# Performance work log

Hardware: AMD Instinct MI355X
Metric: run time of the kernel (lower is better)

## Reference

```python
import jax, jax.numpy as jnp
import numpy as np

N_NODES = 80000; N_EDGES = 480000; F_IN = 5; DIM = 3; HID = 128; LAT = 128
N_POOLS = 2; RATIO = 0.5; SLOPE = 0.2  # GATv2 leaky_relu negative slope


def _p(key, shape, fan_in):
    return jax.random.normal(key, shape, dtype=jnp.float32) / np.sqrt(float(fan_in))


def setup_inputs() -> dict:
    key = jax.random.key(0)
    ks = jax.random.split(key, 20)
    c0 = F_IN + DIM + 3          # conv0 in-channels: x | pos | y*ones
    ch = HID + DIM               # all later convs / pool gnns: h | pos
    return dict(
        x=jax.random.normal(ks[0], (N_NODES, F_IN), dtype=jnp.float32),
        y=jax.random.normal(ks[1], (1,), dtype=jnp.float32),
        pos=jax.random.normal(ks[2], (N_NODES, DIM), dtype=jnp.float32),
        edge_index=jax.random.randint(ks[3], (2, N_EDGES), 0, N_NODES),
        Wl0=_p(ks[4], (c0, HID), c0), Wr0=_p(ks[5], (c0, HID), c0),
        We0=_p(ks[6], (DIM, HID), DIM), a0=_p(ks[7], (HID,), HID), b0=jnp.zeros((HID,), jnp.float32),
        # stacked convs: [conv1, pool-conv1, pool-conv2, last-conv], all (HID+DIM)->HID(=LAT)
        Wls=_p(ks[8], (4, ch, HID), ch), Wrs=_p(ks[9], (4, ch, HID), ch),
        Wes=_p(ks[10], (4, DIM, HID), DIM), atts=_p(ks[11], (4, HID), HID), bs=jnp.zeros((4, HID), jnp.float32),
        # SAGPool score GNNs: (HID+DIM)->1
        pWl=_p(ks[12], (N_POOLS, ch, 1), ch), pWr=_p(ks[13], (N_POOLS, ch, 1), ch),
        pWe=_p(ks[14], (N_POOLS, DIM, 1), DIM), pa=_p(ks[15], (N_POOLS, 1), 1), pb=jnp.zeros((N_POOLS, 1), jnp.float32),
        linW=_p(ks[16], (LAT, LAT), LAT), linb=jnp.zeros((LAT,), jnp.float32),
    )


def _gatv2(xf, ei, ea, Wl, Wr, We, att, b):
    # PyG GATv2Conv, heads=1, add_self_loops=True, fill_value='mean' for loop edge_attr
    N = xf.shape[0]
    src = jnp.asarray(ei[0]); dst = jnp.asarray(ei[1])
    ones = jnp.ones((src.shape[0],), dtype=xf.dtype)
    deg = jax.ops.segment_sum(ones, dst, num_segments=N)
    loop_attr = jax.ops.segment_sum(ea, dst, num_segments=N) / jnp.clip(deg, 1.0)[:, None]
    ar = jnp.arange(N)
    src_f = jnp.concatenate([src, ar]); dst_f = jnp.concatenate([dst, ar])
    ea_f = jnp.concatenate([ea, loop_attr], axis=0)
    xl = xf @ Wl; xr = xf @ Wr                              # [N, C]
    m = jax.nn.leaky_relu(xl[src_f] + xr[dst_f] + ea_f @ We, SLOPE)  # [Ef, C]
    logits = m @ att                                        # [Ef]
    mx = jax.ops.segment_max(logits, dst_f, num_segments=N)
    z = jnp.exp(logits - mx[dst_f])
    denom = jax.ops.segment_sum(z, dst_f, num_segments=N)
    alpha = z / denom[dst_f]
    return jax.ops.segment_sum(alpha[:, None] * xl[src_f], dst_f, num_segments=N) + b


def _augment(ei, N):
    # adj + adj@adj (sparse coo with coalesce): union of 1-hop and 2-hop edges
    s, t = ei[0].astype(np.int64), ei[1].astype(np.int64)
    order = np.argsort(s, kind='stable')
    t2 = t[order]
    counts = np.bincount(s, minlength=N)
    starts = np.concatenate([[0], np.cumsum(counts)[:-1]])
    lens = counts[t]                      # out-degree of each edge's target (middle node)
    total = int(lens.sum())
    within = np.arange(total) - np.repeat(np.cumsum(lens) - lens, lens)
    b = t2[np.repeat(starts[t], lens) + within]
    a = np.repeat(s, lens)
    key = np.unique(np.concatenate([s * N + t, a * N + b]))
    return np.stack([key // N, key % N])


def _filter_adj(ei, perm, N):
    mask = np.zeros(N, dtype=bool); mask[perm] = True
    keep = mask[ei[0]] & mask[ei[1]]
    relabel = np.full(N, -1, dtype=np.int64); relabel[perm] = np.arange(len(perm))
    return relabel[ei[:, keep]]


def _encoder(fl, ei0, structs):
    (x, y, pos, Wl0, Wr0, We0, a0, b0, Wls, Wrs, Wes, atts, bs,
     pWl, pWr, pWe, pa, pb, linW, linb) = fl
    capture = structs is None
    recs = []
    ei = ei0
    ea = pos[ei[1]] - pos[ei[0]]
    h = jax.nn.elu(_gatv2(jnp.concatenate([x, pos, y * jnp.ones_like(pos)], 1), ei, ea, Wl0, Wr0, We0, a0, b0))
    h = jax.nn.elu(_gatv2(jnp.concatenate([h, pos], 1), ei, ea, Wls[0], Wrs[0], Wes[0], atts[0], bs[0]))
    pe = [ei]; pp = [pos]; eas = [ea]
    N = x.shape[0]
    for l in range(N_POOLS):
        ei_aug = _augment(np.asarray(ei), N) if capture else structs[l][0]
        ea_aug = pos[ei_aug[1]] - pos[ei_aug[0]]
        score = jnp.tanh(_gatv2(jnp.concatenate([h, pos], 1), ei_aug, ea_aug,
                                pWl[l], pWr[l], pWe[l], pa[l], pb[l])[:, 0])
        k = int(np.ceil(RATIO * N))
        if capture:
            _, perm = jax.lax.top_k(score, k)
            perm = np.asarray(perm)
            ei_next = _filter_adj(np.asarray(ei), perm, N)
            recs.append((ei_aug, perm, ei_next))
        else:
            _, perm, ei_next = structs[l]
        h = h[perm] * score[perm][:, None]
        pos = pos[perm]
        ei = ei_next; N = k
        ea = pos[ei[1]] - pos[ei[0]]
        pe.insert(0, ei); pp.insert(0, pos); eas.insert(0, ea)
        h = jax.nn.elu(_gatv2(jnp.concatenate([h, pos], 1), ei, ea,
                              Wls[l + 1], Wrs[l + 1], Wes[l + 1], atts[l + 1], bs[l + 1]))
    h = jax.nn.elu(_gatv2(jnp.concatenate([h, pos], 1), ei, ea, Wls[3], Wrs[3], Wes[3], atts[3], bs[3]))
    out = h @ linW + linb   # torch.vmap(self.lin)
    return out, pe, pp, eas, recs


def reference(x, y, pos, edge_index, Wl0, Wr0, We0, a0, b0, Wls, Wrs, Wes, atts, bs,
              pWl, pWr, pWe, pa, pb, linW, linb):
    fl = (x, y, pos, Wl0, Wr0, We0, a0, b0, Wls, Wrs, Wes, atts, bs,
          pWl, pWr, pWe, pa, pb, linW, linb)
    out, pe, pp, eas, _ = _encoder(fl, np.asarray(edge_index), None)
    return (out,) + tuple(jnp.asarray(e) for e in pe) + tuple(pp) + tuple(eas)
```

## Files before the change

### kernel.cpp

```cpp
#include <hip/hip_runtime.h>

typedef unsigned long long ull;

#define NN0 80000
#define EE0 480000
#define KK1 40000
#define KK2 20000
#define FLATMAX 8000000
#define SCH 4096
#define CDIV(a,b) (((a)+(b)-1)/(b))
#define HBINS (1<<21)
#define LSW 1024
#define FCAP 512
#define JCAP 8

#define C_E1 2
#define C_E2 3
#define C_M0 5
#define C_M1 6

__device__ __forceinline__ int getE(const int* p, int s){ if(!p) return s; int e=*p; return e<s? e : s; }
__device__ __forceinline__ float leakyf(float x){ return x>0.f? x : 0.2f*x; }
__device__ __forceinline__ double leakyd(double x){ return x>0.0? x : 0.2*x; }
__device__ __forceinline__ float eluf(float x){ return x>0.f? x : (expf(x)-1.f); }

__device__ __forceinline__ ull encd(double f){ ull u=(ull)__double_as_longlong(f); return (u>>63)? ~u : (u|0x8000000000000000ULL); }

template<int MODE, bool DUAL>
__global__ void gemm_k(const float* __restrict__ F1, const float* __restrict__ pos,
                       const float* __restrict__ yv,
                       const float* __restrict__ W1, const float* __restrict__ W2,
                       const float* __restrict__ bias,
                       float* __restrict__ O1, float* __restrict__ O2, int N)
{
  const int K = MODE==0? 11 : (MODE==1? 131 : 128);
  __shared__ float lf[32][132];
  int t = threadIdx.x;
  int row0 = blockIdx.x*32;

  if(MODE==0){
    for(int i=t;i<32*11;i+=256){
      int r=i/11, k=i-r*11; int row=row0+r;
      float f=0.f;
      if(row<N) f = (k<5)? F1[(size_t)row*5+k] : (k<8? pos[(size_t)row*3+(k-5)] : yv[0]);
      lf[r][k]=f;
    }
  } else {
    for(int i=t;i<32*32;i+=256){
      int r=i>>5, c4=i&31; int row=row0+r;
      float4 v; v.x=0.f;v.y=0.f;v.z=0.f;v.w=0.f;
      if(row<N) v = *(const float4*)(F1+(size_t)row*128+c4*4);
      *(float4*)(&lf[r][c4*4]) = v;
    }
    if(MODE==1){
      for(int i=t;i<32*3;i+=256){
        int r=i/3, d=i-r*3; int row=row0+r;
        lf[r][128+d] = (row<N)? pos[(size_t)row*3+d] : 0.f;
      }
    }
  }
  __syncthreads();

  int cg = t&31, rg = t>>5;
  int g = cg*4;
  int rbase = rg*4;

  float acc1[4][4]; float acc2[4][4];
  #pragma unroll
  for(int rr=0;rr<4;rr++)
    #pragma unroll
    for(int c=0;c<4;c++){ acc1[rr][c]=0.f; acc2[rr][c]=0.f; }

  #pragma unroll 4
  for(int k=0;k<K;k++){
    float4 w = *(const float4*)(W1 + (size_t)k*128 + g);
    float4 v; v.x=0.f;v.y=0.f;v.z=0.f;v.w=0.f;
    if(DUAL) v = *(const float4*)(W2 + (size_t)k*128 + g);
    #pragma unroll
    for(int rr=0;rr<4;rr++){
      float f = lf[rbase+rr][k];
      acc1[rr][0]+=f*w.x; acc1[rr][1]+=f*w.y; acc1[rr][2]+=f*w.z; acc1[rr][3]+=f*w.w;
      if(DUAL){ acc2[rr][0]+=f*v.x; acc2[rr][1]+=f*v.y; acc2[rr][2]+=f*v.z; acc2[rr][3]+=f*v.w; }
    }
  }

  float4 bb; bb.x=0.f;bb.y=0.f;bb.z=0.f;bb.w=0.f;
  if(bias) bb = *(const float4*)(bias+g);
  #pragma unroll
  for(int rr=0;rr<4;rr++){
    int row = row0 + rbase + rr;
    if(row<N){
      float4 r1; r1.x=acc1[rr][0]+bb.x; r1.y=acc1[rr][1]+bb.y; r1.z=acc1[rr][2]+bb.z; r1.w=acc1[rr][3]+bb.w;
      *(float4*)(O1+(size_t)row*128+g) = r1;
      if(DUAL){
        float4 r2; r2.x=acc2[rr][0]; r2.y=acc2[rr][1]; r2.z=acc2[rr][2]; r2.w=acc2[rr][3];
        *(float4*)(O2+(size_t)row*128+g) = r2;
      }
    }
  }
}

__global__ void scan_p1(const int* __restrict__ in, const int* pN, int Ns, int* __restrict__ bsums){
  __shared__ int red[256];
  int n = getE(pN,Ns);
  int base = blockIdx.x*SCH;
  int s=0;
  for(int i=base+threadIdx.x; i<base+SCH; i+=256) if(i<n) s+=in[i];
  red[threadIdx.x]=s; __syncthreads();
  for(int o=128;o;o>>=1){ if(threadIdx.x<(unsigned)o) red[threadIdx.x]+=red[threadIdx.x+o]; __syncthreads(); }
  if(threadIdx.x==0) bsums[blockIdx.x]=red[0];
}
__global__ void scan_p2(int* bsums, int nb){
  __shared__ int lds[256];
  int t=threadIdx.x;
  int v = (t<nb)? bsums[t] : 0;
  lds[t]=v; __syncthreads();
  for(int o=1;o<256;o<<=1){ int u=0; if(t>=o) u=lds[t-o]; __syncthreads(); lds[t]+=u; __syncthreads(); }
  if(t<nb) bsums[t]=lds[t]-v;
}
__global__ void scan_p3(const int* __restrict__ in, int* __restrict__ out, const int* pN, int Ns,
                        const int* __restrict__ bsums, int* total){
  __shared__ int tsum[256];
  int n = getE(pN,Ns);
  int base = blockIdx.x*SCH + threadIdx.x*16;
  int v[16]; int s=0;
  #pragma unroll
  for(int q=0;q<16;q++){ int i=base+q; int xv=(i<n)? in[i]:0; v[q]=s; s+=xv; }
  tsum[threadIdx.x]=s; __syncthreads();
  int mine=s;
  for(int o=1;o<256;o<<=1){ int u=0; if(threadIdx.x>=(unsigned)o) u=tsum[threadIdx.x-o]; __syncthreads(); tsum[threadIdx.x]+=u; __syncthreads(); }
  int pre = bsums[blockIdx.x] + tsum[threadIdx.x] - mine;
  #pragma unroll
  for(int q=0;q<16;q++){
    int i=base+q;
    if(i<=n){
      int val = pre+v[q];
      out[i]=val;
      if(i==n && total) *total=val;
    }
  }
}

__global__ void fscan_p1(const int* __restrict__ es, const int* __restrict__ ed, const int* pE, int Es,
                         const int* __restrict__ rank, int k, int* __restrict__ bsums){
  __shared__ int red[256];
  int n = getE(pE,Es);
  int base = blockIdx.x*SCH;
  int s=0;
  for(int i=base+threadIdx.x; i<base+SCH; i+=256)
    if(i<n) s += (rank[es[i]]<k && rank[ed[i]]<k) ? 1 : 0;
  red[threadIdx.x]=s; __syncthreads();
  for(int o=128;o;o>>=1){ if(threadIdx.x<(unsigned)o) red[threadIdx.x]+=red[threadIdx.x+o]; __syncthreads(); }
  if(threadIdx.x==0) bsums[blockIdx.x]=red[0];
}
__global__ void fscan_p3(const int* __restrict__ es, const int* __restrict__ ed, const int* pE, int Es,
                         const int* __restrict__ rank, int k, const int* __restrict__ bsums,
                         int* __restrict__ ns, int* __restrict__ nd, int* total){
  __shared__ int tsum[256];
  int n = getE(pE,Es);
  int base = blockIdx.x*SCH + threadIdx.x*16;
  int v[16]; int rs[16], rd[16]; unsigned fm=0; int s=0;
  #pragma unroll
  for(int q=0;q<16;q++){
    int i=base+q; int xv=0;
    if(i<n){
      int a=rank[es[i]], b=rank[ed[i]];
      rs[q]=a; rd[q]=b;
      if(a<k && b<k){ xv=1; fm |= 1u<<q; }
    }
    v[q]=s; s+=xv;
  }
  tsum[threadIdx.x]=s; __syncthreads();
  int mine=s;
  for(int o=1;o<256;o<<=1){ int u=0; if(threadIdx.x>=(unsigned)o) u=tsum[threadIdx.x-o]; __syncthreads(); tsum[threadIdx.x]+=u; __syncthreads(); }
  int pre = bsums[blockIdx.x] + tsum[threadIdx.x] - mine;
  #pragma unroll
  for(int q=0;q<16;q++){
    int i=base+q;
    if(i<n && ((fm>>q)&1u)){
      int p = pre+v[q];
      ns[p]=rs[q]; nd[p]=rd[q];
    }
    if(i==n && total) *total = pre+v[q];
  }
}

__global__ void count_src(const int* __restrict__ es, const int* pE, int Es, int* cnts){
  int e = blockIdx.x*256+threadIdx.x; int E = getE(pE,Es); if(e>=E) return;
  atomicAdd(&cnts[es[e]], 1);
}
__global__ void fill_eord(const int* __restrict__ es, const int* __restrict__ ed, const int* pE, int Es,
                          const int* __restrict__ dstarts, int* cursor, int* insrc){
  int e = blockIdx.x*256+threadIdx.x; int E = getE(pE,Es); if(e>=E) return;
  int d = ed[e];
  int p = dstarts[d] + atomicAdd(&cursor[d],1);
  insrc[p] = es[e];
}

__global__ void feat_fused(const int* __restrict__ insrc, const int* __restrict__ dstarts,
                           const float* __restrict__ A, const float* __restrict__ B,
                           const float* __restrict__ pos,
                           const float* __restrict__ We, const float* __restrict__ att,
                           const float* __restrict__ bias, float* __restrict__ h, int N)
{
  __shared__ float lgAll[4][FCAP];
  int wv = threadIdx.x>>6, lane = threadIdx.x&63;
  int w = blockIdx.x*4 + wv;
  bool active = (w<N);
  if(!active) w = N-1;
  float* lg = lgAll[wv];
  int r0=dstarts[w], r1=dstarts[w+1]; int din=r1-r0;
  int c=lane, c2=lane+64;
  float B0 = B[(size_t)w*128+c], B1 = B[(size_t)w*128+c2];
  float We0c=We[c], We1c=We[128+c], We2c=We[256+c];
  float We0d=We[c2], We1d=We[128+c2], We2d=We[256+c2];
  float attc=att[c], attd=att[c2];
  float pw0=pos[w*3], pw1=pos[w*3+1], pw2=pos[w*3+2];

  float ra0[JCAP], ra1[JCAP];
  float l0=0,l1=0,l2=0;
  for(int jb=0;jb<din;jb+=JCAP){
    #pragma unroll
    for(int u=0;u<JCAP;u++){
      int j=jb+u;
      if(j<din){
        int s = insrc[r0+j];
        float e0=pw0-pos[s*3], e1=pw1-pos[s*3+1], e2=pw2-pos[s*3+2];
        l0+=e0; l1+=e1; l2+=e2;
        float a0=A[(size_t)s*128+c], a1=A[(size_t)s*128+c2];
        if(jb==0){ ra0[u]=a0; ra1[u]=a1; }
        float m1 = a0 + B0 + e0*We0c + e1*We1c + e2*We2c;
        float m2 = a1 + B1 + e0*We0d + e1*We1d + e2*We2d;
        float p = leakyf(m1)*attc + leakyf(m2)*attd;
        for(int o=32;o;o>>=1) p += __shfl_down(p,o,64);
        if(lane==0 && j<FCAP) lg[j]=p;
      }
    }
  }
  float inv = 1.f/fmaxf((float)din, 1.f);
  float q0=l0*inv, q1=l1*inv, q2=l2*inv;
  float a0w=A[(size_t)w*128+c], a1w=A[(size_t)w*128+c2];
  float pself;
  {
    float m1 = a0w + B0 + q0*We0c + q1*We1c + q2*We2c;
    float m2 = a1w + B1 + q0*We0d + q1*We1d + q2*We2d;
    float p = leakyf(m1)*attc + leakyf(m2)*attd;
    for(int o=32;o;o>>=1) p += __shfl_down(p,o,64);
    pself = __shfl(p,0,64);
  }
  float mx = pself;
  int dc = din<FCAP? din : FCAP;
  for(int j=lane;j<dc;j+=64) mx = fmaxf(mx, lg[j]);
  for(int o=32;o;o>>=1) mx = fmaxf(mx, __shfl_down(mx,o,64));
  mx = __shfl(mx,0,64);
  for(int j=FCAP;j<din;j++){
    int s = insrc[r0+j];
    float e0=pw0-pos[s*3], e1=pw1-pos[s*3+1], e2=pw2-pos[s*3+2];
    float a0=A[(size_t)s*128+c], a1=A[(size_t)s*128+c2];
    float m1 = a0 + B0 + e0*We0c + e1*We1c + e2*We2c;
    float m2 = a1 + B1 + e0*We0d + e1*We1d + e2*We2d;
    float p = leakyf(m1)*attc + leakyf(m2)*attd;
    for(int o=32;o;o>>=1) p += __shfl_down(p,o,64);
    p = __shfl(p,0,64);
    mx = fmaxf(mx, p);
  }

  float denom=0.f, acc0=0.f, acc1=0.f;
  for(int jb=0;jb<din;jb+=JCAP){
    #pragma unroll
    for(int u=0;u<JCAP;u++){
      int j=jb+u;
      if(j<din){
        float a0,a1; int s=-1;
        if(jb==0){ a0=ra0[u]; a1=ra1[u]; }
        else {
          s = insrc[r0+j];
          a0=A[(size_t)s*128+c]; a1=A[(size_t)s*128+c2];
        }
        float lgj;
        if(j<FCAP) lgj = lg[j];
        else {
          float e0=pw0-pos[s*3], e1=pw1-pos[s*3+1], e2=pw2-pos[s*3+2];
          float m1 = a0 + B0 + e0*We0c + e1*We1c + e2*We2c;
          float m2 = a1 + B1 + e0*We0d + e1*We1d + e2*We2d;
          float p = leakyf(m1)*attc + leakyf(m2)*attd;
          for(int o=32;o;o>>=1) p += __shfl_down(p,o,64);
          lgj = __shfl(p,0,64);
        }
        float z = expf(lgj - mx);
        denom += z;
        acc0 += z*a0;
        acc1 += z*a1;
      }
    }
  }
  {
    float z = expf(pself - mx);
    denom += z;
    acc0 += z*a0w; acc1 += z*a1w;
  }
  float iv = 1.f/denom;
  float b0v=bias[c], b1v=bias[c2];
  acc0 = eluf(acc0*iv + b0v); acc1 = eluf(acc1*iv + b1v);
  if(active){
    h[(size_t)w*128+c ] = acc0;
    h[(size_t)w*128+c2] = acc1;
  }
}

__global__ void gemm_score(const float* __restrict__ h, const float* __restrict__ pos,
                           const float* __restrict__ pWl, const float* __restrict__ pWr,
                           double* __restrict__ xls, double* __restrict__ xrs, int N)
{
  int t = threadIdx.x;
  int lane = t&31;
  int n = blockIdx.x*8 + (t>>5);
  if(n>=N) return;
  double sl=0, sr=0;
  #pragma unroll
  for(int q=0;q<4;q++){
    int k = lane + q*32;
    double f = (double)h[(size_t)n*128+k];
    sl += f*(double)pWl[k]; sr += f*(double)pWr[k];
  }
  if(lane<3){
    double f = (double)pos[n*3+lane];
    sl += f*(double)pWl[128+lane]; sr += f*(double)pWr[128+lane];
  }
  for(int o=16;o;o>>=1){ sl += __shfl_down(sl,o,32); sr += __shfl_down(sr,o,32); }
  if(lane==0){ xls[n]=sl; xrs[n]=sr; }
}

__global__ void score_fused2(const int* __restrict__ insrc, const int* __restrict__ dstarts,
                             const float* __restrict__ pos,
                             const double* __restrict__ xls, const double* __restrict__ xrs,
                             const float* __restrict__ pWe, const float* __restrict__ paP,
                             const float* __restrict__ pbP,
                             double* __restrict__ score, ull* __restrict__ ek, int N)
{
  __shared__ int lsAll[4][LSW];
  int wv = threadIdx.x>>6;
  int lane = threadIdx.x&63;
  int w = blockIdx.x*4 + wv;
  bool active = (w<N);
  if(!active) w = N-1;
  int* ls = lsAll[wv];
  int r0=dstarts[w], r1=dstarts[w+1]; int din=r1-r0;
  for(int j=lane;j<din && j<LSW;j+=64) ls[j]=insrc[r0+j];
  __syncthreads();
  int off = din<LSW? din : LSW;
  for(int base=0; base<din && base<LSW; base+=64){
    int t = base + lane;
    int u0=0, len=0;
    if(t<din && t<LSW){
      int u = ls[t];
      u0 = dstarts[u]; len = dstarts[u+1]-u0;
    }
    int pre = len;
    #pragma unroll
    for(int o=1;o<64;o<<=1){ int v=__shfl_up(pre,o,64); if(lane>=o) pre+=v; }
    int tot = __shfl(pre, 63, 64);
    int myoff = off + pre - len;
    for(int j=0;j<len;j++){ int p=myoff+j; if(p<LSW) ls[p]=insrc[u0+j]; }
    off += tot;
  }
  int d = off<LSW? off : LSW;
  __syncthreads();

  float pd0=pos[w*3], pd1=pos[w*3+1], pd2=pos[w*3+2];
  double w0=(double)pWe[0], w1=(double)pWe[1], w2=(double)pWe[2], pa=(double)paP[0];
  double xrd=xrs[w];
  ull umask=0;
  double lgv[4], xv[4];
  double mx=-1e300, s0=0,s1=0,s2=0; int ucnt=0;
  #pragma unroll
  for(int it=0; it<4; it++){
    int j = lane + it*64;
    if(j<d){
      int s = ls[j];
      bool uniq = true;
      for(int q=0;q<j;q++) if(ls[q]==s){ uniq=false; break; }
      if(uniq){
        umask |= 1ULL<<it;
        ucnt++;
        double e0=(double)(pd0-pos[s*3]), e1=(double)(pd1-pos[s*3+1]), e2=(double)(pd2-pos[s*3+2]);
        s0+=e0; s1+=e1; s2+=e2;
        double xl = xls[s];
        double lg = leakyd(xl+xrd + e0*w0+e1*w1+e2*w2) * pa;
        lgv[it]=lg; xv[it]=xl;
        mx = fmax(mx, lg);
      }
    }
  }
  int nb=4;
  for(int j=lane+256; j<d; j+=64, nb++){
    int s = ls[j];
    bool uniq = true;
    for(int q=0;q<j;q++) if(ls[q]==s){ uniq=false; break; }
    if(uniq){
      umask |= 1ULL<<nb;
      ucnt++;
      double e0=(double)(pd0-pos[s*3]), e1=(double)(pd1-pos[s*3+1]), e2=(double)(pd2-pos[s*3+2]);
      s0+=e0; s1+=e1; s2+=e2;
      double lg = leakyd(xls[s]+xrd + e0*w0+e1*w1+e2*w2) * pa;
      mx = fmax(mx, lg);
    }
  }
  for(int o=32;o;o>>=1){
    mx = fmax(mx, __shfl_down(mx,o,64));
    s0 += __shfl_down(s0,o,64);
    s1 += __shfl_down(s1,o,64);
    s2 += __shfl_down(s2,o,64);
    ucnt += __shfl_down(ucnt,o,64);
  }
  mx=__shfl(mx,0,64); s0=__shfl(s0,0,64); s1=__shfl(s1,0,64); s2=__shfl(s2,0,64); ucnt=__shfl(ucnt,0,64);
  double invd = 1.0/(double)(ucnt>0? ucnt : 1);
  double lg_self = leakyd(xls[w]+xrd + (s0*invd)*w0 + (s1*invd)*w1 + (s2*invd)*w2) * pa;
  mx = fmax(mx, lg_self);
  double den=0, acc=0;
  #pragma unroll
  for(int it=0; it<4; it++){
    if((umask>>it)&1ULL){
      double z = exp(lgv[it]-mx);
      den += z; acc += z*xv[it];
    }
  }
  nb=4;
  for(int j=lane+256; j<d; j+=64, nb++){
    if((umask>>nb)&1ULL){
      int s = ls[j];
      double e0=(double)(pd0-pos[s*3]), e1=(double)(pd1-pos[s*3+1]), e2=(double)(pd2-pos[s*3+2]);
      double lg = leakyd(xls[s]+xrd + e0*w0+e1*w1+e2*w2) * pa;
      double z = exp(lg-mx);
      den += z; acc += z*xls[s];
    }
  }
  for(int o=32;o;o>>=1){
    den += __shfl_down(den,o,64);
    acc += __shfl_down(acc,o,64);
  }
  if(lane==0 && active){
    double z = exp(lg_self-mx);
    den += z; acc += z*xls[w];
    double sc = tanh(acc/den + (double)pbP[0]);
    score[w] = sc;
    ek[w] = encd(sc);
  }
}

__global__ void hist_g(const ull* __restrict__ ek, int N, int shift, const ull* __restrict__ selT,
                       int* __restrict__ hist){
  int i = blockIdx.x*256+threadIdx.x; if(i>=N) return;
  ull key = ek[i];
  if(shift+21 < 64){
    if((key >> (shift+21)) != ((*selT) >> (shift+21))) return;
  }
  atomicAdd(&hist[(int)((key>>shift)&0x1FFFFF)], 1);
}
__global__ void part21(const int* __restrict__ hist, int* __restrict__ partial){
  __shared__ int red[256];
  int b = blockIdx.x;
  int s=0;
  for(int i=threadIdx.x;i<1024;i+=256) s += hist[b*1024+i];
  red[threadIdx.x]=s; __syncthreads();
  for(int o=128;o;o>>=1){ if(threadIdx.x<(unsigned)o) red[threadIdx.x]+=red[threadIdx.x+o]; __syncthreads(); }
  if(threadIdx.x==0) partial[b]=red[0];
}
__global__ void findbin_g(const int* __restrict__ partial, const int* __restrict__ hist,
                          ull* __restrict__ selT, int* __restrict__ selRB, int k, int shift){
  __shared__ int ts[256];
  __shared__ int cstar, rbase;
  int t=threadIdx.x;
  int keff = k - *selRB;
  int s8[8]; int mysum=0;
  #pragma unroll
  for(int q=0;q<8;q++){ s8[q]=partial[t*8+q]; mysum+=s8[q]; }
  ts[t]=mysum; __syncthreads();
  for(int o=1;o<256;o<<=1){ int u=(t+o<256)? ts[t+o]:0; __syncthreads(); ts[t]+=u; __syncthreads(); }
  int after = (t<255)? ts[t+1] : 0;
  if(ts[t] >= keff && after < keff){
    int run = after;
    for(int q=7;q>=0;q--){
      if(run < keff && run + s8[q] >= keff){ cstar = t*8+q; rbase = run; }
      run += s8[q];
    }
  }
  __syncthreads();
  int cs=cstar, rb=rbase;
  int b4[4]; int ms=0;
  #pragma unroll
  for(int q=0;q<4;q++){ b4[q]=hist[cs*1024 + t*4 + q]; ms+=b4[q]; }
  ts[t]=ms; __syncthreads();
  for(int o=1;o<256;o<<=1){ int u=(t+o<256)? ts[t+o]:0; __syncthreads(); ts[t]+=u; __syncthreads(); }
  int after2 = (t<255)? ts[t+1] : 0;
  if(rb+ts[t] >= keff && rb+after2 < keff){
    int run = rb+after2;
    for(int q=3;q>=0;q--){
      if(run < keff && run + b4[q] >= keff){
        *selT |= ((ull)(cs*1024 + t*4 + q)) << shift;
        *selRB = (k - keff) + run;
      }
      run += b4[q];
    }
  }
}
__global__ void rank_hist(const ull* __restrict__ ek, int N, const ull* __restrict__ selT,
                          int* __restrict__ hist){
  int i = blockIdx.x*256+threadIdx.x; if(i>=N) return;
  ull key = ek[i]; if(key < *selT) return;
  int dg = (int)((~key >> 43) & 0x1FFFFF);
  atomicAdd(&hist[dg], 1);
}
__global__ void binscan(const int* __restrict__ hist, const int* __restrict__ p2,
                        int* __restrict__ binstarts){
  __shared__ int ts[256];
  int b = blockIdx.x, t = threadIdx.x;
  int v[4]; int s=0;
  #pragma unroll
  for(int q=0;q<4;q++){ v[q]=s; s+=hist[b*1024 + t*4 + q]; }
  ts[t]=s; __syncthreads();
  int mine=s;
  for(int o=1;o<256;o<<=1){ int u=0; if(t>=(unsigned)o) u=ts[t-o]; __syncthreads(); ts[t]+=u; __syncthreads(); }
  int pre = p2[b] + ts[t] - mine;
  #pragma unroll
  for(int q=0;q<4;q++) binstarts[b*1024 + t*4 + q] = pre + v[q];
  if(b==2047 && t==255) binstarts[HBINS] = p2[b] + ts[255];
}
__global__ void rank_fill(const ull* __restrict__ ek, int N, const ull* __restrict__ selT,
                          const int* __restrict__ binstarts, int* __restrict__ hist,
                          ull* __restrict__ mkeys, int* __restrict__ midx){
  int i = blockIdx.x*256+threadIdx.x; if(i>=N) return;
  ull key = ek[i]; if(key < *selT) return;
  int dg = (int)((~key >> 43) & 0x1FFFFF);
  int o = atomicSub(&hist[dg], 1) - 1;
  int p = binstarts[dg] + o;
  mkeys[p] = key; midx[p] = i;
}
__global__ void rank_within(const int* __restrict__ binstarts,
                            const ull* __restrict__ mkeys, const int* __restrict__ midx,
                            int* __restrict__ rank, int Nmax){
  int m = blockIdx.x*256+threadIdx.x; if(m>=Nmax) return;
  int total = binstarts[HBINS]; if(m>=total) return;
  ull key = mkeys[m]; int ii = midx[m];
  int dg = (int)((~key >> 43) & 0x1FFFFF);
  int s = binstarts[dg], e = binstarts[dg+1];
  int cnt = 0;
  for(int j=s;j<e;j++){
    ull kj = mkeys[j];
    cnt += (kj > key) || (kj == key && midx[j] < ii);
  }
  rank[ii] = s + cnt;
}
__global__ void scatter_perm(const int* __restrict__ rank, int N, int k, int* __restrict__ perm){
  int i = blockIdx.x*256+threadIdx.x; if(i>=N) return;
  int r = rank[i]; if(r<k) perm[r]=i;
}
__global__ void pool_gather(const float* __restrict__ h, const double* __restrict__ score,
                            const int* __restrict__ perm, int k, float* __restrict__ outA){
  int idx = blockIdx.x*256+threadIdx.x; if(idx>=k*32) return;
  int r = idx>>5, g = (idx&31)*4;
  int p = perm[r]; float sc = (float)score[p];
  const float4 x = *(const float4*)(h + (size_t)p*128 + g);
  float4 o; o.x=x.x*sc; o.y=x.y*sc; o.z=x.z*sc; o.w=x.w*sc;
  *(float4*)(outA + (size_t)r*128 + g) = o;
}
__global__ void pos_gather(const float* __restrict__ posc, const int* __restrict__ perm, int k, float* __restrict__ posn){
  int idx = blockIdx.x*256+threadIdx.x; if(idx>=k*3) return;
  int r = idx/3, j = idx-r*3;
  posn[idx] = posc[perm[r]*3+j];
}

__global__ void calc_offsets(const int* __restrict__ cnt, long long* __restrict__ offs){
  if(blockIdx.x==0 && threadIdx.x==0){
    long long E1 = cnt[C_E1], E2 = cnt[C_E2];
    long long o = (long long)KK2*128;
    offs[0]=0;
    offs[1]=o; o += 2*E2;
    offs[2]=o; o += 2*E1;
    offs[3]=o; o += 2*(long long)EE0;
    offs[4]=o; o += (long long)KK2*3;
    offs[5]=o; o += (long long)KK1*3;
    offs[6]=o; o += (long long)NN0*3;
    offs[7]=o; o += 3*E2;
    offs[8]=o; o += 3*E1;
    offs[9]=o;
  }
}
__global__ void emit3_pe(const int* __restrict__ s2, const int* __restrict__ d2, const int* pE2,
                         const int* __restrict__ s1, const int* __restrict__ d1, const int* pE1,
                         const int* __restrict__ s0, const int* __restrict__ d0,
                         const long long* __restrict__ offs, float* __restrict__ out){
  int e = blockIdx.x*256+threadIdx.x;
  int L = blockIdx.y;
  const int* s; const int* d; int E; int oi;
  if(L==0){ s=s2; d=d2; E=getE(pE2,EE0); oi=1; }
  else if(L==1){ s=s1; d=d1; E=getE(pE1,EE0); oi=2; }
  else { s=s0; d=d0; E=EE0; oi=3; }
  if(e>=E) return;
  long long o = offs[oi];
  out[o+e]   = (float)s[e];
  out[o+E+e] = (float)d[e];
}
__global__ void emit3_pp(const float* __restrict__ p2, const float* __restrict__ p1,
                         const float* __restrict__ p0,
                         const long long* __restrict__ offs, float* __restrict__ out){
  int i = blockIdx.x*256+threadIdx.x;
  int L = blockIdx.y;
  const float* p; int n; int oi;
  if(L==0){ p=p2; n=KK2*3; oi=4; }
  else if(L==1){ p=p1; n=KK1*3; oi=5; }
  else { p=p0; n=NN0*3; oi=6; }
  if(i>=n) return;
  out[offs[oi]+i] = p[i];
}
__global__ void emit3_eas(const int* __restrict__ s2, const int* __restrict__ d2, const int* pE2, const float* __restrict__ q2,
                          const int* __restrict__ s1, const int* __restrict__ d1, const int* pE1, const float* __restrict__ q1,
                          const int* __restrict__ s0, const int* __restrict__ d0, const float* __restrict__ q0,
                          const long long* __restrict__ offs, float* __restrict__ out){
  int e = blockIdx.x*256+threadIdx.x;
  int L = blockIdx.y;
  const int* s; const int* d; const float* pos; int E; int oi;
  if(L==0){ s=s2; d=d2; pos=q2; E=getE(pE2,EE0); oi=7; }
  else if(L==1){ s=s1; d=d1; pos=q1; E=getE(pE1,EE0); oi=8; }
  else { s=s0; d=d0; pos=q0; E=EE0; oi=9; }
  if(e>=E) return;
  long long o = offs[oi];
  int ss=s[e], dd=d[e];
  out[o+3*e+0] = pos[dd*3+0]-pos[ss*3+0];
  out[o+3*e+1] = pos[dd*3+1]-pos[ss*3+1];
  out[o+3*e+2] = pos[dd*3+2]-pos[ss*3+2];
}

extern "C" void kernel_launch(void* const* d_in, const int* in_sizes, int n_in,
                              void* d_out, int out_size, void* d_ws, size_t ws_size,
                              hipStream_t stream)
{
  const float* x    = (const float*)d_in[0];
  const float* yv   = (const float*)d_in[1];
  const float* pos0 = (const float*)d_in[2];
  const int*   ei   = (const int*)d_in[3];
  const float* Wl0  = (const float*)d_in[4];
  const float* Wr0  = (const float*)d_in[5];
  const float* We0  = (const float*)d_in[6];
  const float* a0   = (const float*)d_in[7];
  const float* b0   = (const float*)d_in[8];
  const float* Wls  = (const float*)d_in[9];
  const float* Wrs  = (const float*)d_in[10];
  const float* Wes  = (const float*)d_in[11];
  const float* atts = (const float*)d_in[12];
  const float* bs   = (const float*)d_in[13];
  const float* pWl  = (const float*)d_in[14];
  const float* pWr  = (const float*)d_in[15];
  const float* pWe  = (const float*)d_in[16];
  const float* pa   = (const float*)d_in[17];
  const float* pb   = (const float*)d_in[18];
  const float* linW = (const float*)d_in[19];
  const float* linb = (const float*)d_in[20];
  float* out = (float*)d_out;

  const int* eisrc = ei;
  const int* eidst = ei + EE0;

  char* base = (char*)d_ws; size_t off = 0;
  auto alloc = [&](size_t b)->void*{
    off = (off + 255) & ~(size_t)255;
    void* p = base + off; off += b; return p;
  };
  int*       cnt     = (int*)alloc(64*4);
  long long* offs    = (long long*)alloc(16*8);
  int*       bsums   = (int*)alloc(256*4);
  ull*       sel     = (ull*)alloc(2*8);
  int*       hist    = (int*)alloc((size_t)HBINS*4);
  int*       partial = (int*)alloc(2048*4);
  int*       partial2= (int*)alloc(2304*4);
  double*    xls     = (double*)alloc((size_t)NN0*8);
  double*    xrs     = (double*)alloc((size_t)NN0*8);
  double*    score   = (double*)alloc((size_t)NN0*8);
  ull*       ek      = (ull*)alloc((size_t)NN0*8);
  int*       rank    = (int*)alloc((size_t)NN0*4);
  int*       perm    = (int*)alloc((size_t)NN0*4);
  int*       cursor  = (int*)alloc((size_t)NN0*4);
  int*       ccnt    = (int*)alloc((size_t)NN0*4);
  int*       dstarts = (int*)alloc((size_t)(NN0+1)*4);
  int*       insrc   = (int*)alloc((size_t)EE0*4);
  int*       eb0s    = (int*)alloc((size_t)EE0*4);
  int*       eb0d    = (int*)alloc((size_t)EE0*4);
  int*       eb1s    = (int*)alloc((size_t)EE0*4);
  int*       eb1d    = (int*)alloc((size_t)EE0*4);
  float*     pos1    = (float*)alloc((size_t)KK1*12);
  float*     pos2    = (float*)alloc((size_t)KK2*12);
  float*     A       = (float*)alloc((size_t)NN0*128*4);
  float*     B       = (float*)alloc((size_t)NN0*128*4);
  float*     h       = (float*)alloc((size_t)NN0*128*4);
  void*      uni     = alloc((size_t)(EE0+FLATMAX)*8);
  if(off > ws_size) return;

  int*    binstarts= (int*)uni;
  ull*    mkeys    = (ull*)((int*)uni + (HBINS + 256));
  int*    midx     = (int*)(mkeys + NN0);
  ull*    selT  = sel;
  int*    selRB = (int*)(sel+1);

  hipMemsetAsync(cnt, 0, 64*4, stream);
  hipMemsetAsync(hist, 0, (size_t)HBINS*4, stream);

  auto scan = [&](const int* in, int* sout, const int* pN, int Ns, int* total){
    int nb = CDIV(Ns+1, SCH);
    scan_p1<<<nb,256,0,stream>>>(in,pN,Ns,bsums);
    scan_p2<<<1,256,0,stream>>>(bsums,nb);
    scan_p3<<<nb,256,0,stream>>>(in,sout,pN,Ns,bsums,total);
  };

  auto build_csr_dst = [&](const int* es, const int* ed, const int* pE, int Emax, int N){
    hipMemsetAsync(ccnt,0,(size_t)N*4,stream);
    count_src<<<CDIV(Emax,256),256,0,stream>>>(ed,pE,Emax,ccnt);
    scan(ccnt,dstarts,nullptr,N,nullptr);
    hipMemsetAsync(cursor,0,(size_t)N*4,stream);
    fill_eord<<<CDIV(Emax,256),256,0,stream>>>(es,ed,pE,Emax,dstarts,cursor,insrc);
  };

  auto feat_conv = [&](const float* Wl, const float* Wr, const float* We, const float* att, const float* bias,
                       int N, const float* pcur, bool conv0mode){
    if(conv0mode)
      gemm_k<0,true><<<CDIV(N,32),256,0,stream>>>(x,pcur,yv,Wl,Wr,nullptr,A,B,N);
    else
      gemm_k<1,true><<<CDIV(N,32),256,0,stream>>>(h,pcur,nullptr,Wl,Wr,nullptr,A,B,N);
    feat_fused<<<CDIV(N,4),256,0,stream>>>(insrc,dstarts,A,B,pcur,We,att,bias,h,N);
  };

  auto pool = [&](int l, int N, int k, const int* es, const int* ed, const int* pE, int Emax,
                  const float* pcur, float* pnext, int* ns, int* nd, int eslot){
    hipMemsetAsync(rank, 0x3f, (size_t)N*4, stream);
    gemm_score<<<CDIV(N,8),256,0,stream>>>(h,pcur,pWl+l*131,pWr+l*131,xls,xrs,N);
    score_fused2<<<CDIV(N,4),256,0,stream>>>(insrc,dstarts,pcur,xls,xrs,pWe+l*3,pa+l,pb+l,score,ek,N);
    hipMemsetAsync(sel,0,16,stream);
    for(int r=0;r<2;r++){
      int sh = 43 - 21*r;
      if(r>0) hipMemsetAsync(hist,0,(size_t)HBINS*4,stream);
      hist_g<<<CDIV(N,256),256,0,stream>>>(ek,N,sh,selT,hist);
      part21<<<2048,256,0,stream>>>(hist,partial);
      findbin_g<<<1,256,0,stream>>>(partial,hist,selT,selRB,k,sh);
    }
    hipMemsetAsync(hist,0,(size_t)HBINS*4,stream);
    rank_hist  <<<CDIV(N,256),256,0,stream>>>(ek,N,selT,hist);
    part21     <<<2048,256,0,stream>>>(hist,partial);
    scan(partial,partial2,nullptr,2048,nullptr);
    binscan    <<<2048,256,0,stream>>>(hist,partial2,binstarts);
    rank_fill  <<<CDIV(N,256),256,0,stream>>>(ek,N,selT,binstarts,hist,mkeys,midx);
    rank_within<<<CDIV(N,256),256,0,stream>>>(binstarts,mkeys,midx,rank,N);
    scatter_perm<<<CDIV(N,256),256,0,stream>>>(rank,N,k,perm);
    pool_gather<<<CDIV(k*32,256),256,0,stream>>>(h,score,perm,k,A);
    hipMemcpyAsync(h,A,(size_t)k*128*4,hipMemcpyDeviceToDevice,stream);
    pos_gather<<<CDIV(k*3,256),256,0,stream>>>(pcur,perm,k,pnext);
    {
      int nb = CDIV(Emax+1, SCH);
      fscan_p1<<<nb,256,0,stream>>>(es,ed,pE,Emax,rank,k,bsums);
      scan_p2<<<1,256,0,stream>>>(bsums,nb);
      fscan_p3<<<nb,256,0,stream>>>(es,ed,pE,Emax,rank,k,bsums,ns,nd,cnt+eslot);
    }
  };

  build_csr_dst(eisrc,eidst,nullptr,EE0, NN0);
  feat_conv(Wl0,Wr0,We0,a0,b0, NN0, pos0, true);
  feat_conv(Wls+0*16768,Wrs+0*16768,Wes+0*384,atts+0*128,bs+0*128, NN0, pos0, false);
  pool(0, NN0, KK1, eisrc,eidst,nullptr,EE0, pos0,pos1, eb0s,eb0d, C_E1);
  build_csr_dst(eb0s,eb0d,cnt+C_E1,EE0, KK1);
  feat_conv(Wls+1*16768,Wrs+1*16768,Wes+1*384,atts+1*128,bs+1*128, KK1, pos1, false);
  pool(1, KK1, KK2, eb0s,eb0d,cnt+C_E1,EE0, pos1,pos2, eb1s,eb1d, C_E2);
  build_csr_dst(eb1s,eb1d,cnt+C_E2,EE0, KK2);
  feat_conv(Wls+2*16768,Wrs+2*16768,Wes+2*384,atts+2*128,bs+2*128, KK2, pos2, false);
  feat_conv(Wls+3*16768,Wrs+3*16768,Wes+3*384,atts+3*128,bs+3*128, KK2, pos2, false);
  gemm_k<2,false><<<CDIV(KK2,32),256,0,stream>>>(h,nullptr,nullptr,linW,nullptr,linb,out,nullptr,KK2);

  calc_offsets<<<1,32,0,stream>>>(cnt,offs);
  {
    dim3 g(CDIV(EE0,256),3);
    emit3_pe <<<g,256,0,stream>>>(eb1s,eb1d,cnt+C_E2, eb0s,eb0d,cnt+C_E1, eisrc,eidst, offs,out);
    emit3_eas<<<g,256,0,stream>>>(eb1s,eb1d,cnt+C_E2,pos2, eb0s,eb0d,cnt+C_E1,pos1, eisrc,eidst,pos0, offs,out);
  }
  {
    dim3 g(CDIV(NN0*3,256),3);
    emit3_pp <<<g,256,0,stream>>>(pos2,pos1,pos0,offs,out);
  }
}
```

Before: 1.760 ms.

## Reuse first radix histogram for ranking bins and drop pooled-feature copy

The top-k selection now keeps the first-pass 21-bit histogram in its own buffer and uses a second buffer for the refinement pass. The bin-start scan is built directly from that first histogram in reverse order, which removes a separate rank_hist pass, its histogram memset and the multi-kernel scan. The pooled features are written straight into B and the next conv reads from B, so the device-to-device memcpy goes away. In exchange it adds an extra 8 MB histogram buffer, a memset of mkeys, and counts above-threshold items per bin using the full first-pass histogram, which relies on the selT filtering in rank_within to stay correct.

```diff
diff --git a/kernel.cpp b/kernel.cpp
--- a/kernel.cpp
+++ b/kernel.cpp
@@ -504,44 +504,55 @@
     }
   }
 }
-__global__ void rank_hist(const ull* __restrict__ ek, int N, const ull* __restrict__ selT,
-                          int* __restrict__ hist){
-  int i = blockIdx.x*256+threadIdx.x; if(i>=N) return;
-  ull key = ek[i]; if(key < *selT) return;
-  int dg = (int)((~key >> 43) & 0x1FFFFF);
-  atomicAdd(&hist[dg], 1);
-}
-__global__ void binscan(const int* __restrict__ hist, const int* __restrict__ p2,
-                        int* __restrict__ binstarts){
+__global__ void sufscan2048(const int* __restrict__ in, int* __restrict__ outcs){
   __shared__ int ts[256];
-  int b = blockIdx.x, t = threadIdx.x;
+  int t=threadIdx.x;
+  int v[8]; int s=0;
+  #pragma unroll
+  for(int q=7;q>=0;q--){ v[q]=s; s+=in[t*8+q]; }
+  ts[t]=s; __syncthreads();
+  int mine=s;
+  for(int o=1;o<256;o<<=1){ int u=(t+o<256)? ts[t+o]:0; __syncthreads(); ts[t]+=u; __syncthreads(); }
+  int post = ts[t] - mine;
+  #pragma unroll
+  for(int q=0;q<8;q++) outcs[t*8+q] = post + v[q];
+}
+__global__ void binscan_rev(const int* __restrict__ hist1, const int* __restrict__ csum,
+                            int* __restrict__ binstarts){
+  __shared__ int ts[256];
+  int cb = blockIdx.x, t = threadIdx.x;
   int v[4]; int s=0;
   #pragma unroll
-  for(int q=0;q<4;q++){ v[q]=s; s+=hist[b*1024 + t*4 + q]; }
+  for(int q=0;q<4;q++){
+    int ci = cb*1024 + t*4 + q;
+    v[q]=s; s += hist1[HBINS-1-ci];
+  }
   ts[t]=s; __syncthreads();
   int mine=s;
   for(int o=1;o<256;o<<=1){ int u=0; if(t>=(unsigned)o) u=ts[t-o]; __syncthreads(); ts[t]+=u; __syncthreads(); }
-  int pre = p2[b] + ts[t] - mine;
-  #pragma unroll
-  for(int q=0;q<4;q++) binstarts[b*1024 + t*4 + q] = pre + v[q];
-  if(b==2047 && t==255) binstarts[HBINS] = p2[b] + ts[255];
+  int base = csum[2047-cb];
+  int pre = base + ts[t] - mine;
+  #pragma unroll
+  for(int q=0;q<4;q++) binstarts[cb*1024 + t*4 + q] = pre + v[q];
+  if(cb==2047 && t==255) binstarts[HBINS] = csum[0] + ts[255];
 }
 __global__ void rank_fill(const ull* __restrict__ ek, int N, const ull* __restrict__ selT,
-                          const int* __restrict__ binstarts, int* __restrict__ hist,
+                          const int* __restrict__ binstarts, int* __restrict__ hist1,
                           ull* __restrict__ mkeys, int* __restrict__ midx){
   int i = blockIdx.x*256+threadIdx.x; if(i>=N) return;
   ull key = ek[i]; if(key < *selT) return;
-  int dg = (int)((~key >> 43) & 0x1FFFFF);
-  int o = atomicSub(&hist[dg], 1) - 1;
-  int p = binstarts[dg] + o;
+  int dg  = (int)((key >> 43) & 0x1FFFFF);
+  int cdg = 0x1FFFFF - dg;
+  int o = atomicSub(&hist1[dg], 1) - 1;
+  int p = binstarts[cdg] + o;
   mkeys[p] = key; midx[p] = i;
 }
 __global__ void rank_within(const int* __restrict__ binstarts,
                             const ull* __restrict__ mkeys, const int* __restrict__ midx,
-                            int* __restrict__ rank, int Nmax){
+                            const ull* __restrict__ selT, int* __restrict__ rank, int Nmax){
   int m = blockIdx.x*256+threadIdx.x; if(m>=Nmax) return;
-  int total = binstarts[HBINS]; if(m>=total) return;
-  ull key = mkeys[m]; int ii = midx[m];
+  ull key = mkeys[m]; if(key < *selT) return;
+  int ii = midx[m];
   int dg = (int)((~key >> 43) & 0x1FFFFF);
   int s = binstarts[dg], e = binstarts[dg+1];
   int cnt = 0;
@@ -671,7 +682,9 @@
   int*       bsums   = (int*)alloc(256*4);
   ull*       sel     = (ull*)alloc(2*8);
   int*       hist    = (int*)alloc((size_t)HBINS*4);
+  int*       hist2   = (int*)alloc((size_t)HBINS*4);
   int*       partial = (int*)alloc(2048*4);
+  int*       partialB= (int*)alloc(2048*4);
   int*       partial2= (int*)alloc(2304*4);
   double*    xls     = (double*)alloc((size_t)NN0*8);
   double*    xrs     = (double*)alloc((size_t)NN0*8);
@@ -720,37 +733,35 @@
   };
 
   auto feat_conv = [&](const float* Wl, const float* Wr, const float* We, const float* att, const float* bias,
-                       int N, const float* pcur, bool conv0mode){
+                       int N, const float* pcur, const float* hin, bool conv0mode){
     if(conv0mode)
       gemm_k<0,true><<<CDIV(N,32),256,0,stream>>>(x,pcur,yv,Wl,Wr,nullptr,A,B,N);
     else
-      gemm_k<1,true><<<CDIV(N,32),256,0,stream>>>(h,pcur,nullptr,Wl,Wr,nullptr,A,B,N);
+      gemm_k<1,true><<<CDIV(N,32),256,0,stream>>>(hin,pcur,nullptr,Wl,Wr,nullptr,A,B,N);
     feat_fused<<<CDIV(N,4),256,0,stream>>>(insrc,dstarts,A,B,pcur,We,att,bias,h,N);
   };
 
   auto pool = [&](int l, int N, int k, const int* es, const int* ed, const int* pE, int Emax,
                   const float* pcur, float* pnext, int* ns, int* nd, int eslot){
     hipMemsetAsync(rank, 0x3f, (size_t)N*4, stream);
+    if(l>0) hipMemsetAsync(hist, 0, (size_t)HBINS*4, stream);
     gemm_score<<<CDIV(N,8),256,0,stream>>>(h,pcur,pWl+l*131,pWr+l*131,xls,xrs,N);
     score_fused2<<<CDIV(N,4),256,0,stream>>>(insrc,dstarts,pcur,xls,xrs,pWe+l*3,pa+l,pb+l,score,ek,N);
     hipMemsetAsync(sel,0,16,stream);
-    for(int r=0;r<2;r++){
-      int sh = 43 - 21*r;
-      if(r>0) hipMemsetAsync(hist,0,(size_t)HBINS*4,stream);
-      hist_g<<<CDIV(N,256),256,0,stream>>>(ek,N,sh,selT,hist);
-      part21<<<2048,256,0,stream>>>(hist,partial);
-      findbin_g<<<1,256,0,stream>>>(partial,hist,selT,selRB,k,sh);
-    }
-    hipMemsetAsync(hist,0,(size_t)HBINS*4,stream);
-    rank_hist  <<<CDIV(N,256),256,0,stream>>>(ek,N,selT,hist);
-    part21     <<<2048,256,0,stream>>>(hist,partial);
-    scan(partial,partial2,nullptr,2048,nullptr);
-    binscan    <<<2048,256,0,stream>>>(hist,partial2,binstarts);
+    hist_g<<<CDIV(N,256),256,0,stream>>>(ek,N,43,selT,hist);
+    part21<<<2048,256,0,stream>>>(hist,partial);
+    findbin_g<<<1,256,0,stream>>>(partial,hist,selT,selRB,k,43);
+    hipMemsetAsync(hist2,0,(size_t)HBINS*4,stream);
+    hist_g<<<CDIV(N,256),256,0,stream>>>(ek,N,22,selT,hist2);
+    part21<<<2048,256,0,stream>>>(hist2,partialB);
+    findbin_g<<<1,256,0,stream>>>(partialB,hist2,selT,selRB,k,22);
+    hipMemsetAsync(mkeys,0,(size_t)N*8,stream);
+    sufscan2048<<<1,256,0,stream>>>(partial,partial2);
+    binscan_rev<<<2048,256,0,stream>>>(hist,partial2,binstarts);
     rank_fill  <<<CDIV(N,256),256,0,stream>>>(ek,N,selT,binstarts,hist,mkeys,midx);
-    rank_within<<<CDIV(N,256),256,0,stream>>>(binstarts,mkeys,midx,rank,N);
+    rank_within<<<CDIV(N,256),256,0,stream>>>(binstarts,mkeys,midx,selT,rank,N);
     scatter_perm<<<CDIV(N,256),256,0,stream>>>(rank,N,k,perm);
-    pool_gather<<<CDIV(k*32,256),256,0,stream>>>(h,score,perm,k,A);
-    hipMemcpyAsync(h,A,(size_t)k*128*4,hipMemcpyDeviceToDevice,stream);
+    pool_gather<<<CDIV(k*32,256),256,0,stream>>>(h,score,perm,k,B);
     pos_gather<<<CDIV(k*3,256),256,0,stream>>>(pcur,perm,k,pnext);
     {
       int nb = CDIV(Emax+1, SCH);
@@ -761,15 +772,15 @@
   };
 
   build_csr_dst(eisrc,eidst,nullptr,EE0, NN0);
-  feat_conv(Wl0,Wr0,We0,a0,b0, NN0, pos0, true);
-  feat_conv(Wls+0*16768,Wrs+0*16768,Wes+0*384,atts+0*128,bs+0*128, NN0, pos0, false);
+  feat_conv(Wl0,Wr0,We0,a0,b0, NN0, pos0, nullptr, true);
+  feat_conv(Wls+0*16768,Wrs+0*16768,Wes+0*384,atts+0*128,bs+0*128, NN0, pos0, h, false);
   pool(0, NN0, KK1, eisrc,eidst,nullptr,EE0, pos0,pos1, eb0s,eb0d, C_E1);
   build_csr_dst(eb0s,eb0d,cnt+C_E1,EE0, KK1);
-  feat_conv(Wls+1*16768,Wrs+1*16768,Wes+1*384,atts+1*128,bs+1*128, KK1, pos1, false);
+  feat_conv(Wls+1*16768,Wrs+1*16768,Wes+1*384,atts+1*128,bs+1*128, KK1, pos1, B, false);
   pool(1, KK1, KK2, eb0s,eb0d,cnt+C_E1,EE0, pos1,pos2, eb1s,eb1d, C_E2);
   build_csr_dst(eb1s,eb1d,cnt+C_E2,EE0, KK2);
-  feat_conv(Wls+2*16768,Wrs+2*16768,Wes+2*384,atts+2*128,bs+2*128, KK2, pos2, false);
-  feat_conv(Wls+3*16768,Wrs+3*16768,Wes+3*384,atts+3*128,bs+3*128, KK2, pos2, false);
+  feat_conv(Wls+2*16768,Wrs+2*16768,Wes+2*384,atts+2*128,bs+2*128, KK2, pos2, B, false);
+  feat_conv(Wls+3*16768,Wrs+3*16768,Wes+3*384,atts+3*128,bs+3*128, KK2, pos2, h, false);
   gemm_k<2,false><<<CDIV(KK2,32),256,0,stream>>>(h,nullptr,nullptr,linW,nullptr,linb,out,nullptr,KK2);
 
   calc_offsets<<<1,32,0,stream>>>(cnt,offs);
```

Measured after the change: 1.651 ms (median of 2 runs). 1.07x faster.
